# Kernel tuning notes

Hardware: AMD Instinct MI355X
Metric: run time of the kernel (lower is better)

The kernel has to match this reference:

```python
import jax, jax.numpy as jnp
import numpy as np

B, T, C, H, O = 64, 256, 2048, 512, 11
THRESHOLD = 1.0
LEAK = 0.003
OUTPUT_LEAK = LEAK * 0.5


def setup_inputs() -> dict:
    key = jax.random.key(0)
    k1, k2, k3, k4 = jax.random.split(key, 4)
    x = jax.random.normal(k1, (B, T, C), dtype=jnp.float32)
    # xavier_uniform(gain=0.1) for fc1: bound = 0.1*sqrt(6/(C+H))
    b1 = 0.1 * np.sqrt(6.0 / (C + H))
    w1 = jax.random.uniform(k2, (H, C), jnp.float32, -b1, b1)
    # orthogonal(gain=0.1) for fc_rec -> approximate with small gaussian scaled like orthogonal rows
    w_rec = 0.1 * jnp.linalg.qr(jax.random.normal(k3, (H, H), jnp.float32))[0]
    b2 = 0.3 * np.sqrt(6.0 / (H + O))
    w2 = jax.random.uniform(k4, (O, H), jnp.float32, -b2, b2)
    return {"x": x, "w1": w1, "w_rec": w_rec, "w2": w2}


def reference(x, w1, w_rec, w2):
    batch, t_steps, _ = x.shape
    n_hidden = w1.shape[0]
    n_output = w2.shape[0]
    dt = x.dtype

    def step(carry, x_t):
        v1, spk1, v2, out_sum = carry
        # input + recurrent current: [B,H]
        i1 = x_t @ w1.T + spk1 @ w_rec.T
        # subtractive LIF: leak, threshold, subtractive reset
        v1 = v1 + i1 - LEAK
        spk = (v1 >= THRESHOLD).astype(dt)
        v1 = v1 - spk * THRESHOLD
        # non-spiking output accumulator neuron: [B,O]
        i2 = spk @ w2.T
        v2 = jnp.maximum(v2 + i2 - OUTPUT_LEAK, 0.0)
        out_sum = out_sum + v2
        return (v1, spk, v2, out_sum), None

    init = (
        jnp.zeros((batch, n_hidden), dt),
        jnp.zeros((batch, n_hidden), dt),
        jnp.zeros((batch, n_output), dt),
        jnp.zeros((batch, n_output), dt),
    )
    (_, _, _, out_sum), _ = jax.lax.scan(step, init, jnp.swapaxes(x, 0, 1))
    return out_sum / t_steps
```

## Files before the change

### kernel.cpp

```cpp
#include <hip/hip_runtime.h>
#include <cstddef>

#define B_ 64
#define T_ 256
#define C_ 2048
#define H_ 512
#define O_ 11
#define THRESH 1.0f
#define LEAK_ 0.003f
#define OLEAK_ 0.0015f

typedef float v2f __attribute__((ext_vector_type(2)));

__device__ __forceinline__ void lds_barrier() {
    asm volatile("s_waitcnt lgkmcnt(0)" ::: "memory");
    __builtin_amdgcn_s_barrier();
}

__global__ __launch_bounds__(256) void transpose_wrec(const float* __restrict__ w,
                                                      float* __restrict__ wt) {
    __shared__ float tile[32][33];
    int tx = threadIdx.x, ty = threadIdx.y;
    int x = blockIdx.x * 32 + tx;
    int y = blockIdx.y * 32 + ty;
#pragma unroll
    for (int i = 0; i < 32; i += 8)
        tile[ty + i][tx] = w[(size_t)(y + i) * H_ + x];
    __syncthreads();
    int x2 = blockIdx.y * 32 + tx;
    int y2 = blockIdx.x * 32 + ty;
#pragma unroll
    for (int i = 0; i < 32; i += 8)
        wt[(size_t)(y2 + i) * H_ + x2] = tile[tx][ty + i];
}

#define BM 128
#define BN 128
#define BK 16
#define LDT (BM + 4)

template <int S>
__global__ __launch_bounds__(256) void gemm_ff(const float* __restrict__ A,
                                               const float* __restrict__ Bw,
                                               float* __restrict__ Pout) {
    const int K = C_;
    const int N = H_;
    const int kLen = C_ / S;

    const int i  = blockIdx.x + 4 * blockIdx.y + 512 * blockIdx.z;
    const int l  = (i & 7) * (64 * S) + (i >> 3);
    const int bx = l & 3;
    const int by = (l >> 2) & 127;
    const int bz = l >> 9;
    const int kBase = bz * kLen;

    __shared__ float As[2][BK][LDT];
    __shared__ float Bs[2][BK][LDT];

    const int t  = threadIdx.x;
    const int tx = t & 15;
    const int ty = t >> 4;
    const int lr = t >> 2;
    const int lc = (t & 3) * 4;

    const float* Ap = A  + (size_t)(by * BM + lr) * K + kBase + lc;
    const float* Bp = Bw + (size_t)(bx * BN + lr) * K + kBase + lc;

    v2f acc[8][4];
#pragma unroll
    for (int ii = 0; ii < 8; ++ii)
#pragma unroll
        for (int j = 0; j < 4; ++j) acc[ii][j] = (v2f){0.f, 0.f};

    float4 a0 = *(const float4*)(Ap);
    float4 a1 = *(const float4*)(Ap + (size_t)64 * K);
    float4 b0 = *(const float4*)(Bp);
    float4 b1 = *(const float4*)(Bp + (size_t)64 * K);

    auto stage = [&](int pb) {
        As[pb][lc + 0][lr] = a0.x; As[pb][lc + 1][lr] = a0.y;
        As[pb][lc + 2][lr] = a0.z; As[pb][lc + 3][lr] = a0.w;
        As[pb][lc + 0][lr + 64] = a1.x; As[pb][lc + 1][lr + 64] = a1.y;
        As[pb][lc + 2][lr + 64] = a1.z; As[pb][lc + 3][lr + 64] = a1.w;
        Bs[pb][lc + 0][lr] = b0.x; Bs[pb][lc + 1][lr] = b0.y;
        Bs[pb][lc + 2][lr] = b0.z; Bs[pb][lc + 3][lr] = b0.w;
        Bs[pb][lc + 0][lr + 64] = b1.x; Bs[pb][lc + 1][lr + 64] = b1.y;
        Bs[pb][lc + 2][lr + 64] = b1.z; Bs[pb][lc + 3][lr + 64] = b1.w;
    };

    auto compute = [&](int pb) {
#pragma unroll
        for (int k = 0; k < BK; ++k) {
            float4 alo = *(const float4*)&As[pb][k][ty * 4];
            float4 ahi = *(const float4*)&As[pb][k][64 + ty * 4];
            float4 blo = *(const float4*)&Bs[pb][k][tx * 4];
            float4 bhi = *(const float4*)&Bs[pb][k][64 + tx * 4];
            v2f b0v = {blo.x, blo.y}, b1v = {blo.z, blo.w};
            v2f b2v = {bhi.x, bhi.y}, b3v = {bhi.z, bhi.w};
            float av[8] = {alo.x, alo.y, alo.z, alo.w, ahi.x, ahi.y, ahi.z, ahi.w};
#pragma unroll
            for (int ii = 0; ii < 8; ++ii) {
                v2f ai = {av[ii], av[ii]};
                acc[ii][0] += ai * b0v;
                acc[ii][1] += ai * b1v;
                acc[ii][2] += ai * b2v;
                acc[ii][3] += ai * b3v;
            }
        }
    };

    stage(0);
    __syncthreads();

    int p = 0;
    for (int k0 = BK; k0 < kLen; k0 += BK) {
        Ap += BK; Bp += BK;
        a0 = *(const float4*)(Ap);
        a1 = *(const float4*)(Ap + (size_t)64 * K);
        b0 = *(const float4*)(Bp);
        b1 = *(const float4*)(Bp + (size_t)64 * K);
        compute(p);
        stage(p ^ 1);
        lds_barrier();
        p ^= 1;
    }
    compute(p);

    float* P = Pout + (size_t)bz * ((size_t)B_ * T_ * H_);
#pragma unroll
    for (int ii = 0; ii < 8; ++ii) {
        int row = by * BM + (ii < 4 ? ty * 4 + ii : 64 + ty * 4 + (ii - 4));
        float* Cp = P + (size_t)row * N + bx * BN;
        float4 c0 = {acc[ii][0].x, acc[ii][0].y, acc[ii][1].x, acc[ii][1].y};
        float4 c1 = {acc[ii][2].x, acc[ii][2].y, acc[ii][3].x, acc[ii][3].y};
        *(float4*)(Cp + tx * 4)      = c0;
        *(float4*)(Cp + 64 + tx * 4) = c1;
    }
}

template <int S>
__global__ __launch_bounds__(512) void snn_rec(const float* __restrict__ I1,
                                               const float* __restrict__ wrT,
                                               const float* __restrict__ w2,
                                               float* __restrict__ out) {
    const int b    = blockIdx.x;
    const int h    = threadIdx.x;
    const int lane = h & 63;
    const int w    = h >> 6;

    __shared__ float w2sT[H_ * 12];
    __shared__ int   lists[2][H_];
    __shared__ int   wcnt[8];
    __shared__ float v2s[O_];
    __shared__ float osum[O_];

#pragma unroll
    for (int o = 0; o < O_; ++o) w2sT[h * 12 + o] = w2[o * H_ + h];
    if (h < O_) { v2s[h] = 0.f; osum[h] = 0.f; }

    float v1 = 0.f;
    int   pc = 0;
    const float*  i1p  = I1 + (size_t)b * T_ * H_ + h;
    const float*  wr_h = wrT + h;
    const size_t  PARTF = (size_t)B_ * T_ * H_;

    float pf[S];
#pragma unroll
    for (int s = 0; s < S; ++s) pf[s] = i1p[s * PARTF];
    __syncthreads();

    for (int t = 0; t < T_; ++t) {
        const int cur = t & 1;

        float acc = -LEAK_;
#pragma unroll
        for (int s = 0; s < S; ++s) acc += pf[s];

        const int tn = (t + 1 < T_) ? t + 1 : t;
#pragma unroll
        for (int s = 0; s < S; ++s) pf[s] = i1p[s * PARTF + (size_t)tn * H_];

        const int* pl = lists[cur ^ 1];
        int j = 0;
        for (; j + 15 < pc; j += 16) {
            const int4 ia = *(const int4*)(pl + j);
            const int4 ib = *(const int4*)(pl + j + 4);
            const int4 ic = *(const int4*)(pl + j + 8);
            const int4 id = *(const int4*)(pl + j + 12);
            float g0 = wr_h[ia.x * H_], g1 = wr_h[ia.y * H_];
            float g2 = wr_h[ia.z * H_], g3 = wr_h[ia.w * H_];
            float g4 = wr_h[ib.x * H_], g5 = wr_h[ib.y * H_];
            float g6 = wr_h[ib.z * H_], g7 = wr_h[ib.w * H_];
            float g8 = wr_h[ic.x * H_], g9 = wr_h[ic.y * H_];
            float gA = wr_h[ic.z * H_], gB = wr_h[ic.w * H_];
            float gC = wr_h[id.x * H_], gD = wr_h[id.y * H_];
            float gE = wr_h[id.z * H_], gF = wr_h[id.w * H_];
            acc += g0; acc += g1; acc += g2; acc += g3;
            acc += g4; acc += g5; acc += g6; acc += g7;
            acc += g8; acc += g9; acc += gA; acc += gB;
            acc += gC; acc += gD; acc += gE; acc += gF;
        }
        for (; j + 7 < pc; j += 8) {
            const int4 ia = *(const int4*)(pl + j);
            const int4 ib = *(const int4*)(pl + j + 4);
            float g0 = wr_h[ia.x * H_], g1 = wr_h[ia.y * H_];
            float g2 = wr_h[ia.z * H_], g3 = wr_h[ia.w * H_];
            float g4 = wr_h[ib.x * H_], g5 = wr_h[ib.y * H_];
            float g6 = wr_h[ib.z * H_], g7 = wr_h[ib.w * H_];
            acc += g0; acc += g1; acc += g2; acc += g3;
            acc += g4; acc += g5; acc += g6; acc += g7;
        }
        for (; j < pc; ++j) acc += wr_h[pl[j] * H_];

        v1 += acc;
        const bool spike = (v1 >= THRESH);
        if (spike) v1 -= THRESH;

        unsigned long long m = __ballot(spike);
        int lb = __popcll(m & ((1ull << lane) - 1ull));
        if (lane == 0) wcnt[w] = (int)__popcll(m);
        lds_barrier();

        int base = 0, tot = 0;
#pragma unroll
        for (int ww = 0; ww < 8; ++ww) {
            int c = wcnt[ww];
            if (ww < w) base += c;
            tot += c;
        }
        if (spike) lists[cur][base + lb] = h;
        lds_barrier();

        if (h < O_) {
            const int* cl = lists[cur];
            float s2 = 0.f;
            for (int j2 = 0; j2 < tot; ++j2) s2 += w2sT[cl[j2] * 12 + h];
            float v2 = v2s[h] + s2 - OLEAK_;
            v2 = v2 > 0.f ? v2 : 0.f;
            v2s[h] = v2;
            osum[h] += v2;
        }
        pc = tot;
    }
    __syncthreads();
    if (h < O_) out[b * O_ + h] = osum[h] * (1.0f / (float)T_);
}

extern "C" void kernel_launch(void* const* d_in, const int* in_sizes, int n_in,
                              void* d_out, int out_size, void* d_ws, size_t ws_size,
                              hipStream_t stream) {
    const float* x     = (const float*)d_in[0];
    const float* w1    = (const float*)d_in[1];
    const float* w_rec = (const float*)d_in[2];
    const float* w2    = (const float*)d_in[3];
    float* out = (float*)d_out;

    const size_t PART = (size_t)B_ * T_ * H_ * sizeof(float);
    const size_t WRT  = (size_t)H_ * H_ * sizeof(float);

    int S = 1;
    if (ws_size >= 4 * PART + WRT) S = 4;
    else if (ws_size >= 2 * PART + WRT) S = 2;

    float* P   = (float*)d_ws;
    float* wrT = (float*)((char*)d_ws + (size_t)S * PART);

    transpose_wrec<<<dim3(H_ / 32, H_ / 32), dim3(32, 8), 0, stream>>>(w_rec, wrT);

    dim3 ggrid(H_ / BN, (B_ * T_) / BM, S);
    switch (S) {
        case 4:
            gemm_ff<4><<<ggrid, dim3(256), 0, stream>>>(x, w1, P);
            snn_rec<4><<<dim3(B_), dim3(H_), 0, stream>>>(P, wrT, w2, out);
            break;
        case 2:
            gemm_ff<2><<<ggrid, dim3(256), 0, stream>>>(x, w1, P);
            snn_rec<2><<<dim3(B_), dim3(H_), 0, stream>>>(P, wrT, w2, out);
            break;
        default:
            gemm_ff<1><<<ggrid, dim3(256), 0, stream>>>(x, w1, P);
            snn_rec<1><<<dim3(B_), dim3(H_), 0, stream>>>(P, wrT, w2, out);
            break;
    }
}
```

Measured before the change: 744.2 us.

## Run recurrent SNN scan with one wavefront per batch using ballot spike masks

The recurrent kernel now uses a single 64-lane wavefront per batch row, and each lane owns 8 hidden neurons. Spike lists built in LDS with two block barriers per step are replaced by per-wave ballot bitmasks walked with ctz. Each spiking neuron's weight row is read as 8 coalesced loads, one per 64-column slice. This removes all block-level synchronisation and LDS list traffic from the serial time loop. The cost is far fewer threads in flight (64 waves on the whole GPU), so the scan relies on per-lane ILP to hide the gather latency.

```diff
diff --git a/kernel.cpp b/kernel.cpp
--- a/kernel.cpp
+++ b/kernel.cpp
@@ -139,111 +139,94 @@
 }
 
 template <int S>
-__global__ __launch_bounds__(512) void snn_rec(const float* __restrict__ I1,
-                                               const float* __restrict__ wrT,
-                                               const float* __restrict__ w2,
-                                               float* __restrict__ out) {
-    const int b    = blockIdx.x;
-    const int h    = threadIdx.x;
-    const int lane = h & 63;
-    const int w    = h >> 6;
+__global__ __launch_bounds__(64) void snn_rec(const float* __restrict__ I1,
+                                              const float* __restrict__ wrT,
+                                              const float* __restrict__ w2,
+                                              float* __restrict__ out) {
+    const int b = blockIdx.x;
+    const int l = threadIdx.x;
+    const size_t PARTF = (size_t)B_ * T_ * H_;
 
     __shared__ float w2sT[H_ * 12];
-    __shared__ int   lists[2][H_];
-    __shared__ int   wcnt[8];
-    __shared__ float v2s[O_];
-    __shared__ float osum[O_];
-
-#pragma unroll
-    for (int o = 0; o < O_; ++o) w2sT[h * 12 + o] = w2[o * H_ + h];
-    if (h < O_) { v2s[h] = 0.f; osum[h] = 0.f; }
-
-    float v1 = 0.f;
-    int   pc = 0;
-    const float*  i1p  = I1 + (size_t)b * T_ * H_ + h;
-    const float*  wr_h = wrT + h;
-    const size_t  PARTF = (size_t)B_ * T_ * H_;
-
-    float pf[S];
-#pragma unroll
-    for (int s = 0; s < S; ++s) pf[s] = i1p[s * PARTF];
+    for (int k = l; k < H_; k += 64)
+#pragma unroll
+        for (int o = 0; o < O_; ++o) w2sT[k * 12 + o] = w2[o * H_ + k];
     __syncthreads();
 
+    float v1[8];
+#pragma unroll
+    for (int r = 0; r < 8; ++r) v1[r] = 0.f;
+    float v2 = 0.f, osum = 0.f;
+    unsigned long long pmask[8];
+#pragma unroll
+    for (int r = 0; r < 8; ++r) pmask[r] = 0ull;
+
+    const unsigned off0 = (unsigned)(b * T_ * H_) + (unsigned)l;
+
+    float pf[S][8];
+#pragma unroll
+    for (int s = 0; s < S; ++s)
+#pragma unroll
+        for (int r = 0; r < 8; ++r)
+            pf[s][r] = I1[(size_t)s * PARTF + off0 + r * 64];
+
     for (int t = 0; t < T_; ++t) {
-        const int cur = t & 1;
-
-        float acc = -LEAK_;
-#pragma unroll
-        for (int s = 0; s < S; ++s) acc += pf[s];
-
-        const int tn = (t + 1 < T_) ? t + 1 : t;
-#pragma unroll
-        for (int s = 0; s < S; ++s) pf[s] = i1p[s * PARTF + (size_t)tn * H_];
-
-        const int* pl = lists[cur ^ 1];
-        int j = 0;
-        for (; j + 15 < pc; j += 16) {
-            const int4 ia = *(const int4*)(pl + j);
-            const int4 ib = *(const int4*)(pl + j + 4);
-            const int4 ic = *(const int4*)(pl + j + 8);
-            const int4 id = *(const int4*)(pl + j + 12);
-            float g0 = wr_h[ia.x * H_], g1 = wr_h[ia.y * H_];
-            float g2 = wr_h[ia.z * H_], g3 = wr_h[ia.w * H_];
-            float g4 = wr_h[ib.x * H_], g5 = wr_h[ib.y * H_];
-            float g6 = wr_h[ib.z * H_], g7 = wr_h[ib.w * H_];
-            float g8 = wr_h[ic.x * H_], g9 = wr_h[ic.y * H_];
-            float gA = wr_h[ic.z * H_], gB = wr_h[ic.w * H_];
-            float gC = wr_h[id.x * H_], gD = wr_h[id.y * H_];
-            float gE = wr_h[id.z * H_], gF = wr_h[id.w * H_];
-            acc += g0; acc += g1; acc += g2; acc += g3;
-            acc += g4; acc += g5; acc += g6; acc += g7;
-            acc += g8; acc += g9; acc += gA; acc += gB;
-            acc += gC; acc += gD; acc += gE; acc += gF;
-        }
-        for (; j + 7 < pc; j += 8) {
-            const int4 ia = *(const int4*)(pl + j);
-            const int4 ib = *(const int4*)(pl + j + 4);
-            float g0 = wr_h[ia.x * H_], g1 = wr_h[ia.y * H_];
-            float g2 = wr_h[ia.z * H_], g3 = wr_h[ia.w * H_];
-            float g4 = wr_h[ib.x * H_], g5 = wr_h[ib.y * H_];
-            float g6 = wr_h[ib.z * H_], g7 = wr_h[ib.w * H_];
-            acc += g0; acc += g1; acc += g2; acc += g3;
-            acc += g4; acc += g5; acc += g6; acc += g7;
-        }
-        for (; j < pc; ++j) acc += wr_h[pl[j] * H_];
-
-        v1 += acc;
-        const bool spike = (v1 >= THRESH);
-        if (spike) v1 -= THRESH;
-
-        unsigned long long m = __ballot(spike);
-        int lb = __popcll(m & ((1ull << lane) - 1ull));
-        if (lane == 0) wcnt[w] = (int)__popcll(m);
-        lds_barrier();
-
-        int base = 0, tot = 0;
-#pragma unroll
-        for (int ww = 0; ww < 8; ++ww) {
-            int c = wcnt[ww];
-            if (ww < w) base += c;
-            tot += c;
-        }
-        if (spike) lists[cur][base + lb] = h;
-        lds_barrier();
-
-        if (h < O_) {
-            const int* cl = lists[cur];
+        float acc[8];
+#pragma unroll
+        for (int r = 0; r < 8; ++r) {
+            acc[r] = -LEAK_;
+#pragma unroll
+            for (int s = 0; s < S; ++s) acc[r] += pf[s][r];
+        }
+
+        const unsigned offn = off0 + (unsigned)(((t + 1 < T_) ? t + 1 : t) * H_);
+#pragma unroll
+        for (int s = 0; s < S; ++s)
+#pragma unroll
+            for (int r = 0; r < 8; ++r)
+                pf[s][r] = I1[(size_t)s * PARTF + offn + r * 64];
+
+#pragma unroll
+        for (int w = 0; w < 8; ++w) {
+            unsigned long long m = pmask[w];
+            while (m) {
+                const int idx = (w << 6) + (int)__builtin_ctzll(m);
+                m &= m - 1;
+                const float* row = wrT + (size_t)idx * H_ + l;
+                float g0 = row[0 * 64], g1 = row[1 * 64];
+                float g2 = row[2 * 64], g3 = row[3 * 64];
+                float g4 = row[4 * 64], g5 = row[5 * 64];
+                float g6 = row[6 * 64], g7 = row[7 * 64];
+                acc[0] += g0; acc[1] += g1; acc[2] += g2; acc[3] += g3;
+                acc[4] += g4; acc[5] += g5; acc[6] += g6; acc[7] += g7;
+            }
+        }
+
+#pragma unroll
+        for (int r = 0; r < 8; ++r) {
+            v1[r] += acc[r];
+            const bool sp = (v1[r] >= THRESH);
+            if (sp) v1[r] -= THRESH;
+            pmask[r] = __ballot(sp);
+        }
+
+        if (l < O_) {
             float s2 = 0.f;
-            for (int j2 = 0; j2 < tot; ++j2) s2 += w2sT[cl[j2] * 12 + h];
-            float v2 = v2s[h] + s2 - OLEAK_;
-            v2 = v2 > 0.f ? v2 : 0.f;
-            v2s[h] = v2;
-            osum[h] += v2;
-        }
-        pc = tot;
-    }
-    __syncthreads();
-    if (h < O_) out[b * O_ + h] = osum[h] * (1.0f / (float)T_);
+#pragma unroll
+            for (int w = 0; w < 8; ++w) {
+                unsigned long long m = pmask[w];
+                while (m) {
+                    const int idx = (w << 6) + (int)__builtin_ctzll(m);
+                    m &= m - 1;
+                    s2 += w2sT[idx * 12 + l];
+                }
+            }
+            float nv2 = v2 + s2 - OLEAK_;
+            v2 = nv2 > 0.f ? nv2 : 0.f;
+            osum += v2;
+        }
+    }
+    if (l < O_) out[b * O_ + l] = osum * (1.0f / (float)T_);
 }
 
 extern "C" void kernel_launch(void* const* d_in, const int* in_sizes, int n_in,
@@ -271,15 +254,15 @@
     switch (S) {
         case 4:
             gemm_ff<4><<<ggrid, dim3(256), 0, stream>>>(x, w1, P);
-            snn_rec<4><<<dim3(B_), dim3(H_), 0, stream>>>(P, wrT, w2, out);
+            snn_rec<4><<<dim3(B_), dim3(64), 0, stream>>>(P, wrT, w2, out);
             break;
         case 2:
             gemm_ff<2><<<ggrid, dim3(256), 0, stream>>>(x, w1, P);
-            snn_rec<2><<<dim3(B_), dim3(H_), 0, stream>>>(P, wrT, w2, out);
+            snn_rec<2><<<dim3(B_), dim3(64), 0, stream>>>(P, wrT, w2, out);
             break;
         default:
             gemm_ff<1><<<ggrid, dim3(256), 0, stream>>>(x, w1, P);
-            snn_rec<1><<<dim3(B_), dim3(H_), 0, stream>>>(P, wrT, w2, out);
+            snn_rec<1><<<dim3(B_), dim3(64), 0, stream>>>(P, wrT, w2, out);
             break;
     }
 }
```

Measured after the change: 741.1 us. No clear change (-0.4%).
